# Optimization experiments

Hardware: AMD Instinct MI355X
Metric: run time of the kernel (lower is better)

The kernel has to match this reference:

```python
import jax, jax.numpy as jnp
import numpy as np

N = 16384          # input points
F = 128            # feature dim (x is (N, 3+F))
POOL = 4           # pooling_factor
M = N // POOL      # number of FPS query points
K = 16             # num_neighbors


def setup_inputs() -> dict:
    key = jax.random.key(0)
    x = jax.random.normal(key, (N, 3 + F), dtype=jnp.float32)
    return {"x": x}


def _fps(coords, m):
    """Furthest point sampling: coords (N,3) -> m indices. Deterministic start at 0."""
    n = coords.shape[0]

    def step(carry, _):
        min_d2, last = carry
        d2 = jnp.sum((coords - coords[last]) ** 2, axis=-1)  # (N,)
        min_d2 = jnp.minimum(min_d2, d2)
        nxt = jnp.argmax(min_d2).astype(jnp.int32)
        return (min_d2, nxt), nxt

    init = (jnp.full((n,), jnp.inf, dtype=coords.dtype), jnp.int32(0))
    _, idxs = jax.lax.scan(step, init, None, length=m - 1)
    return jnp.concatenate([jnp.zeros((1,), dtype=jnp.int32), idxs])


def reference(x):
    coords = x[:, :3]                          # (N,3)
    fps_idx = _fps(coords, M)                  # (M,)
    q_points = coords[fps_idx]                 # (M,3)

    # knn neighbor query: squared distances (M,N), take K nearest
    d2 = jnp.sum((q_points[:, None, :] - coords[None, :, :]) ** 2, axis=-1)
    _, nbr_idx = jax.lax.top_k(-d2, K)         # (M,K)

    s_feats = x[nbr_idx, 3:]                   # (M,K,F) gather
    pooled = jnp.max(s_feats, axis=1)          # feat_mapping='max' -> (M,F)
    return jnp.concatenate([q_points, pooled], axis=-1)  # (M, 3+F)
```

## Files before the change

### kernel.cpp

```cpp
#include <hip/hip_runtime.h>

#define N_PTS 16384
#define ROWF  131
#define M_OUT 4096
#define KNN   16
#define FPS_T 1024
#define CHUNK 16
#define SORT_T 1024

typedef unsigned long long u64;

__device__ __constant__ unsigned short c_spread4[16] =
  {0,1,8,9,64,65,72,73,512,513,520,521,576,577,584,585};

__device__ __forceinline__ int cell_of(float x, float y, float z) {
  int ix = (int)floorf((x + 4.0f) * 2.0f); ix = ix < 0 ? 0 : (ix > 15 ? 15 : ix);
  int iy = (int)floorf((y + 4.0f) * 2.0f); iy = iy < 0 ? 0 : (iy > 15 ? 15 : iy);
  int iz = (int)floorf((z + 4.0f) * 2.0f); iz = iz < 0 ? 0 : (iz > 15 ? 15 : iz);
  return (int)c_spread4[ix] | ((int)c_spread4[iy] << 1) | ((int)c_spread4[iz] << 2);
}

__global__ void prep_kernel(const float* __restrict__ x,
                            float* __restrict__ cX, float* __restrict__ cY,
                            float* __restrict__ cZ) {
  const int p = blockIdx.x * blockDim.x + threadIdx.x;
  if (p < N_PTS) {
    cX[p] = x[p * ROWF + 0];
    cY[p] = x[p * ROWF + 1];
    cZ[p] = x[p * ROWF + 2];
  }
}

__global__ __launch_bounds__(1024, 1)
void sort_kernel(const float* __restrict__ cX, const float* __restrict__ cY,
                 const float* __restrict__ cZ, float4* __restrict__ gP4) {
  __shared__ unsigned int sh[4096];
  __shared__ unsigned int sws[16];
  const int tid = threadIdx.x, lane = tid & 63, wid = tid >> 6;

#pragma unroll
  for (int i = 0; i < 4; ++i) sh[tid * 4 + i] = 0;
  __syncthreads();

  int cel[16];
#pragma unroll
  for (int j = 0; j < 16; ++j) {
    const int p = tid + SORT_T * j;
    const int c = cell_of(cX[p], cY[p], cZ[p]);
    cel[j] = c;
    atomicAdd(&sh[c], 1u);
  }
  __syncthreads();

  const unsigned h0 = sh[tid * 4 + 0], h1 = sh[tid * 4 + 1];
  const unsigned h2 = sh[tid * 4 + 2], h3 = sh[tid * 4 + 3];
  const unsigned tsum = h0 + h1 + h2 + h3;
  unsigned inc = tsum;
#pragma unroll
  for (int off = 1; off < 64; off <<= 1) {
    const unsigned v = __shfl_up(inc, off);
    if (lane >= off) inc += v;
  }
  if (lane == 63) sws[wid] = inc;
  __syncthreads();
  if (tid == 0) {
    unsigned run = 0;
#pragma unroll
    for (int w = 0; w < 16; ++w) { const unsigned t = sws[w]; sws[w] = run; run += t; }
  }
  __syncthreads();
  const unsigned base = sws[wid] + inc - tsum;
  sh[tid * 4 + 0] = base;
  sh[tid * 4 + 1] = base + h0;
  sh[tid * 4 + 2] = base + h0 + h1;
  sh[tid * 4 + 3] = base + h0 + h1 + h2;
  __syncthreads();

#pragma unroll
  for (int j = 0; j < 16; ++j) {
    const int p = tid + SORT_T * j;
    const unsigned rk = atomicAdd(&sh[cel[j]], 1u);
    const int slot = ((rk & 15) << 10) | (int)(rk >> 4);
    gP4[slot] = make_float4(cX[p], cY[p], cZ[p], __int_as_float(p));
  }
}

__global__ __launch_bounds__(FPS_T, 4)
void fps_kernel(const float* __restrict__ cX, const float* __restrict__ cY,
                const float* __restrict__ cZ, const float4* __restrict__ gP4,
                float* __restrict__ out, float* __restrict__ qc) {
  __shared__ u64 s_wkey[2][16];
  const int tid = threadIdx.x, lane = tid & 63, wid = tid >> 6;

  float px[CHUNK], py[CHUNK], pz[CHUNK], md[CHUNK];
  unsigned ni[CHUNK];

#pragma unroll
  for (int j = 0; j < CHUNK; ++j) {
    const float4 v = gP4[(j << 10) + tid];
    px[j] = v.x; py[j] = v.y; pz[j] = v.z;
    ni[j] = (unsigned)(N_PTS - 1 - __float_as_int(v.w));
    md[j] = __int_as_float(0x7f800000);
  }

  float sx = 0.f, sy = 0.f, sz = 0.f;
#pragma unroll
  for (int j = 0; j < CHUNK; ++j) { sx += px[j]; sy += py[j]; sz += pz[j]; }
  const float mx = sx * (1.0f / CHUNK), my = sy * (1.0f / CHUNK),
              mz = sz * (1.0f / CHUNK);
  float r2 = 0.f;
#pragma unroll
  for (int j = 0; j < CHUNK; ++j) {
    const float dx = px[j] - mx, dy = py[j] - my, dz = pz[j] - mz;
    r2 = fmaxf(r2, dx * dx + dy * dy + dz * dz);
  }
  const float r = sqrtf(r2) * 1.000001f + 1e-6f;

  float cmax = __int_as_float(0x7f800000);
  u64 ckey = 0;

  float qx = cX[0], qy = cY[0], qz = cZ[0];
  if (tid == 0) {
    out[0] = qx; out[1] = qy; out[2] = qz;
    qc[0] = qx; qc[1] = qy; qc[2] = qz;
  }

  for (int s = 1; s < M_OUT; ++s) {
    const float ddx = mx - qx, ddy = my - qy, ddz = mz - qz;
    const float dd = ddx * ddx + ddy * ddy + ddz * ddz;
    const float lb = sqrtf(dd) * 0.999999f - r;
    const bool skip = (lb > 0.f) && (lb * lb >= cmax * 1.0001f + 1e-12f);

    if (!skip) {
      u64 nk = 0;
#pragma unroll
      for (int j = 0; j < CHUNK; ++j) {
        const float dx = px[j] - qx, dy = py[j] - qy, dz = pz[j] - qz;
        const float d2 = __fadd_rn(__fadd_rn(__fmul_rn(dx, dx),
                                             __fmul_rn(dy, dy)),
                                   __fmul_rn(dz, dz));
        const float nm = fminf(md[j], d2);
        md[j] = nm;
        const u64 kj = ((u64)__float_as_uint(nm) << 32) | ni[j];
        nk = (kj > nk) ? kj : nk;
      }
      ckey = nk;
      cmax = __uint_as_float((unsigned)(nk >> 32));
    }

    u64 k = ckey;
#pragma unroll
    for (int off = 32; off; off >>= 1) {
      const u64 o = __shfl_xor(k, off);
      if (o > k) k = o;
    }
    const int par = s & 1;
    if (lane == 0) s_wkey[par][wid] = k;
    __syncthreads();
    u64 kk = s_wkey[par][lane & 15];
#pragma unroll
    for (int off = 8; off; off >>= 1) {
      const u64 o = __shfl_xor(kk, off);
      if (o > kk) kk = o;
    }
    const int oidx = (N_PTS - 1) - (int)(unsigned)kk;
    qx = cX[oidx]; qy = cY[oidx]; qz = cZ[oidx];
    if (tid == 0) {
      float* orow = out + (size_t)s * ROWF;
      orow[0] = qx; orow[1] = qy; orow[2] = qz;
      qc[s * 3 + 0] = qx; qc[s * 3 + 1] = qy; qc[s * 3 + 2] = qz;
    }
  }
}

__global__ __launch_bounds__(256)
void knn_pool_kernel(const float* __restrict__ x,
                     const float* __restrict__ cX, const float* __restrict__ cY,
                     const float* __restrict__ cZ,
                     const float* __restrict__ qc, float* __restrict__ out) {
  const int lane = threadIdx.x & 63;
  const int q = blockIdx.x * 4 + (threadIdx.x >> 6);

  const float qx = qc[q * 3 + 0], qy = qc[q * 3 + 1], qz = qc[q * 3 + 2];

  u64 h[KNN];
#pragma unroll
  for (int k = 0; k < KNN; ++k) h[k] = ~0ULL;

  for (int c = lane; c < N_PTS; c += 64) {
    const float dx = cX[c] - qx, dy = cY[c] - qy, dz = cZ[c] - qz;
    const float d2 = __fadd_rn(__fadd_rn(__fmul_rn(dx, dx), __fmul_rn(dy, dy)),
                               __fmul_rn(dz, dz));
    const u64 e = ((u64)__float_as_uint(d2) << 32) | (unsigned)c;
    if (e < h[KNN - 1]) {
#pragma unroll
      for (int k = KNN - 1; k >= 1; --k) {
        const u64 prev = h[k - 1];
        h[k] = (e < prev) ? prev : ((e < h[k]) ? e : h[k]);
      }
      h[0] = (e < h[0]) ? e : h[0];
    }
  }

  int nbr[KNN];
#pragma unroll
  for (int rr = 0; rr < KNN; ++rr) {
    u64 best = h[0];
#pragma unroll
    for (int off = 32; off; off >>= 1) {
      const u64 o = __shfl_xor(best, off);
      best = (o < best) ? o : best;
    }
    nbr[rr] = (int)(unsigned)(best & 0xffffffffULL);
    if (h[0] == best) {
#pragma unroll
      for (int k = 0; k < KNN - 1; ++k) h[k] = h[k + 1];
      h[KNN - 1] = ~0ULL;
    }
  }

  float a0 = __int_as_float(0xff800000), a1 = a0;
#pragma unroll
  for (int rr = 0; rr < KNN; ++rr) {
    const float* row = x + (size_t)nbr[rr] * ROWF + 3;
    a0 = fmaxf(a0, row[lane]);
    a1 = fmaxf(a1, row[lane + 64]);
  }
  float* orow = out + (size_t)q * ROWF + 3;
  orow[lane] = a0;
  orow[lane + 64] = a1;
}

extern "C" void kernel_launch(void* const* d_in, const int* in_sizes, int n_in,
                              void* d_out, int out_size, void* d_ws, size_t ws_size,
                              hipStream_t stream) {
  const float* x = (const float*)d_in[0];
  float* out = (float*)d_out;

  float*  cX  = (float*)d_ws;
  float*  cY  = cX + N_PTS;
  float*  cZ  = cY + N_PTS;
  float4* gP4 = (float4*)(cZ + N_PTS);
  float*  qc  = (float*)(gP4 + N_PTS);

  hipLaunchKernelGGL(prep_kernel, dim3(16), dim3(1024), 0, stream, x, cX, cY, cZ);
  hipLaunchKernelGGL(sort_kernel, dim3(1), dim3(1024), 0, stream, cX, cY, cZ, gP4);
  hipLaunchKernelGGL(fps_kernel, dim3(1), dim3(FPS_T), 0, stream,
                     cX, cY, cZ, gP4, out, qc);
  hipLaunchKernelGGL(knn_pool_kernel, dim3(M_OUT / 4), dim3(256), 0, stream,
                     x, cX, cY, cZ, qc, out);
}
```

Baseline: 7.428 ms.

## Pack coordinates as float4, simplify FPS skip bound, drop query-coord buffer

Replaces the three separate SoA coordinate arrays with one float4 array, so each point's coordinates come from a single vector load in the sort, FPS and kNN kernels. The FPS cluster-skip test is rewritten to precompute a squared upper bound once, when the chunk is refreshed, which takes a sqrt and several multiplies off every iteration's serial path. kNN now reads the query coordinates back from the output rows, so the qc buffer and its stores go away. It also drops the FPS min-blocks launch bound and changes the prep launch shape. The new skip bound relies on slightly different conservative margins, so rounding at the edges could in principle change which chunks get skipped.

Result: faster. 7.275 ms (-2.1%).

```diff
diff --git a/kernel.cpp b/kernel.cpp
--- a/kernel.cpp
+++ b/kernel.cpp
@@ -21,19 +21,16 @@
 }
 
 __global__ void prep_kernel(const float* __restrict__ x,
-                            float* __restrict__ cX, float* __restrict__ cY,
-                            float* __restrict__ cZ) {
+                            float4* __restrict__ coords4) {
   const int p = blockIdx.x * blockDim.x + threadIdx.x;
   if (p < N_PTS) {
-    cX[p] = x[p * ROWF + 0];
-    cY[p] = x[p * ROWF + 1];
-    cZ[p] = x[p * ROWF + 2];
+    coords4[p] = make_float4(x[p * ROWF + 0], x[p * ROWF + 1],
+                             x[p * ROWF + 2], 0.0f);
   }
 }
 
 __global__ __launch_bounds__(1024, 1)
-void sort_kernel(const float* __restrict__ cX, const float* __restrict__ cY,
-                 const float* __restrict__ cZ, float4* __restrict__ gP4) {
+void sort_kernel(const float4* __restrict__ coords4, float4* __restrict__ gP4) {
   __shared__ unsigned int sh[4096];
   __shared__ unsigned int sws[16];
   const int tid = threadIdx.x, lane = tid & 63, wid = tid >> 6;
@@ -45,8 +42,8 @@
   int cel[16];
 #pragma unroll
   for (int j = 0; j < 16; ++j) {
-    const int p = tid + SORT_T * j;
-    const int c = cell_of(cX[p], cY[p], cZ[p]);
+    const float4 v = coords4[tid + SORT_T * j];
+    const int c = cell_of(v.x, v.y, v.z);
     cel[j] = c;
     atomicAdd(&sh[c], 1u);
   }
@@ -79,16 +76,16 @@
 #pragma unroll
   for (int j = 0; j < 16; ++j) {
     const int p = tid + SORT_T * j;
+    const float4 v = coords4[p];
     const unsigned rk = atomicAdd(&sh[cel[j]], 1u);
-    const int slot = ((rk & 15) << 10) | (int)(rk >> 4);
-    gP4[slot] = make_float4(cX[p], cY[p], cZ[p], __int_as_float(p));
-  }
-}
-
-__global__ __launch_bounds__(FPS_T, 4)
-void fps_kernel(const float* __restrict__ cX, const float* __restrict__ cY,
-                const float* __restrict__ cZ, const float4* __restrict__ gP4,
-                float* __restrict__ out, float* __restrict__ qc) {
+    const int slot = (int)(((rk & 15u) << 10) | (rk >> 4));
+    gP4[slot] = make_float4(v.x, v.y, v.z, __int_as_float(p));
+  }
+}
+
+__global__ __launch_bounds__(FPS_T)
+void fps_kernel(const float4* __restrict__ coords4,
+                const float4* __restrict__ gP4, float* __restrict__ out) {
   __shared__ u64 s_wkey[2][16];
   const int tid = threadIdx.x, lane = tid & 63, wid = tid >> 6;
 
@@ -116,20 +113,17 @@
   }
   const float r = sqrtf(r2) * 1.000001f + 1e-6f;
 
-  float cmax = __int_as_float(0x7f800000);
+  float u2 = __int_as_float(0x7f800000);
   u64 ckey = 0;
 
-  float qx = cX[0], qy = cY[0], qz = cZ[0];
-  if (tid == 0) {
-    out[0] = qx; out[1] = qy; out[2] = qz;
-    qc[0] = qx; qc[1] = qy; qc[2] = qz;
-  }
+  const float4 q0 = coords4[0];
+  float qx = q0.x, qy = q0.y, qz = q0.z;
+  if (tid == 0) { out[0] = qx; out[1] = qy; out[2] = qz; }
 
   for (int s = 1; s < M_OUT; ++s) {
     const float ddx = mx - qx, ddy = my - qy, ddz = mz - qz;
     const float dd = ddx * ddx + ddy * ddy + ddz * ddz;
-    const float lb = sqrtf(dd) * 0.999999f - r;
-    const bool skip = (lb > 0.f) && (lb * lb >= cmax * 1.0001f + 1e-12f);
+    const bool skip = (dd * 0.999999f > u2);
 
     if (!skip) {
       u64 nk = 0;
@@ -145,7 +139,9 @@
         nk = (kj > nk) ? kj : nk;
       }
       ckey = nk;
-      cmax = __uint_as_float((unsigned)(nk >> 32));
+      const float cmax = __uint_as_float((unsigned)(nk >> 32));
+      const float u = (sqrtf(cmax * 1.0001f + 1e-12f) + r) * 1.000003f;
+      u2 = u * u * 1.000001f;
     }
 
     u64 k = ckey;
@@ -164,31 +160,33 @@
       if (o > kk) kk = o;
     }
     const int oidx = (N_PTS - 1) - (int)(unsigned)kk;
-    qx = cX[oidx]; qy = cY[oidx]; qz = cZ[oidx];
+    const float4 w = coords4[oidx];
+    qx = w.x; qy = w.y; qz = w.z;
     if (tid == 0) {
       float* orow = out + (size_t)s * ROWF;
       orow[0] = qx; orow[1] = qy; orow[2] = qz;
-      qc[s * 3 + 0] = qx; qc[s * 3 + 1] = qy; qc[s * 3 + 2] = qz;
     }
   }
 }
 
 __global__ __launch_bounds__(256)
 void knn_pool_kernel(const float* __restrict__ x,
-                     const float* __restrict__ cX, const float* __restrict__ cY,
-                     const float* __restrict__ cZ,
-                     const float* __restrict__ qc, float* __restrict__ out) {
+                     const float4* __restrict__ coords4,
+                     float* __restrict__ out) {
   const int lane = threadIdx.x & 63;
   const int q = blockIdx.x * 4 + (threadIdx.x >> 6);
 
-  const float qx = qc[q * 3 + 0], qy = qc[q * 3 + 1], qz = qc[q * 3 + 2];
+  const float qx = out[(size_t)q * ROWF + 0];
+  const float qy = out[(size_t)q * ROWF + 1];
+  const float qz = out[(size_t)q * ROWF + 2];
 
   u64 h[KNN];
 #pragma unroll
   for (int k = 0; k < KNN; ++k) h[k] = ~0ULL;
 
   for (int c = lane; c < N_PTS; c += 64) {
-    const float dx = cX[c] - qx, dy = cY[c] - qy, dz = cZ[c] - qz;
+    const float4 v = coords4[c];
+    const float dx = v.x - qx, dy = v.y - qy, dz = v.z - qz;
     const float d2 = __fadd_rn(__fadd_rn(__fmul_rn(dx, dx), __fmul_rn(dy, dy)),
                                __fmul_rn(dz, dz));
     const u64 e = ((u64)__float_as_uint(d2) << 32) | (unsigned)c;
@@ -237,16 +235,13 @@
   const float* x = (const float*)d_in[0];
   float* out = (float*)d_out;
 
-  float*  cX  = (float*)d_ws;
-  float*  cY  = cX + N_PTS;
-  float*  cZ  = cY + N_PTS;
-  float4* gP4 = (float4*)(cZ + N_PTS);
-  float*  qc  = (float*)(gP4 + N_PTS);
-
-  hipLaunchKernelGGL(prep_kernel, dim3(16), dim3(1024), 0, stream, x, cX, cY, cZ);
-  hipLaunchKernelGGL(sort_kernel, dim3(1), dim3(1024), 0, stream, cX, cY, cZ, gP4);
+  float4* coords4 = (float4*)d_ws;
+  float4* gP4     = coords4 + N_PTS;
+
+  hipLaunchKernelGGL(prep_kernel, dim3(64), dim3(256), 0, stream, x, coords4);
+  hipLaunchKernelGGL(sort_kernel, dim3(1), dim3(1024), 0, stream, coords4, gP4);
   hipLaunchKernelGGL(fps_kernel, dim3(1), dim3(FPS_T), 0, stream,
-                     cX, cY, cZ, gP4, out, qc);
+                     coords4, gP4, out);
   hipLaunchKernelGGL(knn_pool_kernel, dim3(M_OUT / 4), dim3(256), 0, stream,
-                     x, cX, cY, cZ, qc, out);
-}
+                     x, coords4, out);
+}
```
